# Kernel tuning notes

Hardware: AMD Instinct MI355X
Metric: run time of the kernel (lower is better)

The kernel has to match this reference:

```python
import jax, jax.numpy as jnp
import numpy as np


def binarize_ste(W):
    # sign binarization with straight-through estimator:
    # forward = sign(W) (zeros mapped to +1, standard BNN convention),
    # backward = identity.
    s = jnp.where(W >= 0, 1.0, -1.0).astype(W.dtype)
    return W + jax.lax.stop_gradient(s - W)


def setup_inputs() -> dict:
    key = jax.random.key(0)
    k1, k2 = jax.random.split(key)
    B, N_IN, N_UNITS = 4096, 4096, 4096
    x = jax.random.normal(k1, (B, N_IN), dtype=jnp.float32)
    W = jax.random.normal(k2, (N_IN, N_UNITS), dtype=jnp.float32) * 0.1  # truncated_normal(stddev=0.1) analog
    b = jnp.zeros((N_UNITS,), dtype=jnp.float32)  # constant_initializer(0.0)
    return {"x": x, "W": W, "b": b}


def reference(x, W, b):
    bin_w = binarize_ste(W)           # [n_in, n_units], values in {-1, +1}
    out = x @ bin_w + b               # dense GEMM + bias
    return jax.nn.relu(out)           # act
```

## Files before the change

kernel.cpp:

```cpp
#include <hip/hip_runtime.h>
#include <hip/hip_bf16.h>

typedef unsigned short u16;
typedef signed char i8;
typedef __attribute__((ext_vector_type(4))) int   int4v;
typedef __attribute__((ext_vector_type(4))) float f32x4;

#define GLOBAL_AS __attribute__((address_space(1)))
#define LDS_AS    __attribute__((address_space(3)))

__device__ __forceinline__ void gload_lds16(const void* g, void* l) {
    __builtin_amdgcn_global_load_lds((const GLOBAL_AS unsigned int*)g,
                                     (LDS_AS unsigned int*)l, 16, 0, 0);
}

__global__ __launch_bounds__(256) void quant_x_kernel(const float* __restrict__ X,
                                                      i8* __restrict__ Xq,
                                                      float* __restrict__ inv_s) {
    const int row = blockIdx.x;
    const int t   = threadIdx.x;
    const float4* src = (const float4*)(X + (size_t)row * 4096 + t * 16);
    float4 v0 = src[0], v1 = src[1], v2 = src[2], v3 = src[3];
    float vals[16] = {v0.x, v0.y, v0.z, v0.w, v1.x, v1.y, v1.z, v1.w,
                      v2.x, v2.y, v2.z, v2.w, v3.x, v3.y, v3.z, v3.w};
    float m = 0.f;
#pragma unroll
    for (int j = 0; j < 16; ++j) m = fmaxf(m, fabsf(vals[j]));
#pragma unroll
    for (int off = 32; off; off >>= 1) m = fmaxf(m, __shfl_xor(m, off));
    __shared__ float sm[4];
    if ((t & 63) == 0) sm[t >> 6] = m;
    __syncthreads();
    m = fmaxf(fmaxf(sm[0], sm[1]), fmaxf(sm[2], sm[3]));
    const float s = (m > 0.f) ? 127.0f / m : 0.f;
    uint4 packed;
    unsigned int* pw = (unsigned int*)&packed;
#pragma unroll
    for (int g = 0; g < 4; ++g) {
        unsigned int wd = 0;
#pragma unroll
        for (int j = 0; j < 4; ++j) {
            int q = (int)rintf(vals[g * 4 + j] * s);
            wd |= ((unsigned int)(q & 255)) << (8 * j);
        }
        pw[g] = wd;
    }
    ((uint4*)(Xq + (size_t)row * 4096))[t] = packed;
    if (t == 0) inv_s[row] = m * (1.0f / 127.0f);
}

__global__ __launch_bounds__(256) void conv_w_kernel(const float* __restrict__ W,
                                                     i8* __restrict__ Wt) {
    __shared__ __attribute__((aligned(16))) i8 tile[64][80];
    const int t  = threadIdx.x;
    const int k0 = (blockIdx.x & 63) * 64;
    const int n0 = (blockIdx.x >> 6) * 64;
#pragma unroll
    for (int i = 0; i < 4; ++i) {
        const int r = i * 16 + (t >> 4);
        const int c = (t & 15) * 4;
        float4 v = *(const float4*)&W[(size_t)(k0 + r) * 4096 + n0 + c];
        tile[c + 0][r] = (v.x >= 0.f) ? 1 : -1;
        tile[c + 1][r] = (v.y >= 0.f) ? 1 : -1;
        tile[c + 2][r] = (v.z >= 0.f) ? 1 : -1;
        tile[c + 3][r] = (v.w >= 0.f) ? 1 : -1;
    }
    __syncthreads();
    const int r = t >> 2;
    const int c = (t & 3) * 16;
    *(int4*)&Wt[(size_t)(n0 + r) * 4096 + k0 + c] = *(const int4*)&tile[r][c];
}


#define BAR()        __builtin_amdgcn_s_barrier()
#define LGKM0M()     asm volatile("s_waitcnt lgkmcnt(0)" ::: "memory")
#define WAIT_VM6()   asm volatile("s_waitcnt vmcnt(6)" ::: "memory")

#define STAGE_TILE(bufb, koff)                                                      \
    do {                                                                            \
        gload_lds16(AsrcT + (koff),                     lds + (bufb) + wA);         \
        gload_lds16(AsrcT + 65536 + (koff),             lds + (bufb) + wA + 1024);  \
        gload_lds16(BsrcT + (koff),                     lds + (bufb) + 8192 + wB);          \
        gload_lds16(BsrcT + 65536 + (koff),             lds + (bufb) + 8192 + wB + 1024);   \
        gload_lds16(BsrcT + 131072 + (koff),            lds + (bufb) + 8192 + wB + 2048);   \
        gload_lds16(BsrcT + 196608 + (koff),            lds + (bufb) + 8192 + wB + 3072);   \
    } while (0)

__global__ __launch_bounds__(256, 2) void gemm_bin_kernel(const i8* __restrict__ A,
                                                          const i8* __restrict__ Bt,
                                                          const float* __restrict__ bias,
                                                          const float* __restrict__ inv_s,
                                                          float* __restrict__ C) {
    __shared__ __attribute__((aligned(1024))) char lds[49152];

    const int bid = blockIdx.x;
    const int swz = (bid & 7) * 64 + (bid >> 3);
    const int bm  = swz >> 4;
    const int bn  = swz & 15;

    const int tid = threadIdx.x;
    const int w   = tid >> 6;
    const int l   = tid & 63;
    const int wm  = w >> 1;
    const int wn  = w & 1;

    const int lin8 = (l & 7) ^ (l >> 3);
    const int sr2  = (l >> 3) * 2 + (lin8 >> 2);
    const int sc   = (lin8 & 3) * 16;
    const char* AsrcT = (const char*)A  + (size_t)(bm * 128 + 32 * w + sr2) * 4096 + sc;
    const char* BsrcT = (const char*)Bt + (size_t)(bn * 256 + 64 * w + sr2) * 4096 + sc;
    const int wA = w * 2048;
    const int wB = w * 4096;

    const int rsl  = ((l >> 4) + 4 * (l & 1)) ^ ((l >> 1) & 7);
    const int a_rd = wm * 4096 + ((l & 15) >> 1) * 128 + rsl * 16;
    const int b_rd = 8192 + wn * 8192 + ((l & 15) >> 1) * 128 + rsl * 16;

    int4v acc[4][8] = {};
    int4v af[4], bf[8];

    STAGE_TILE(0, 0);
    STAGE_TILE(24576, 64);
    WAIT_VM6();
    BAR();

    for (int t = 0; t < 64; ++t) {
        const int bufb  = (t & 1) * 24576;
        const int koff2 = ((t + 2) & 63) * 64;

#pragma unroll
        for (int mi = 0; mi < 4; ++mi)
            af[mi] = *(const int4v*)(lds + bufb + a_rd + mi * 1024);
#pragma unroll
        for (int ni = 0; ni < 8; ++ni)
            bf[ni] = *(const int4v*)(lds + bufb + b_rd + ni * 1024);
        LGKM0M();
        BAR();
        STAGE_TILE(bufb, koff2);
        WAIT_VM6();
        BAR();

        __builtin_amdgcn_s_setprio(1);
#pragma unroll
        for (int mi = 0; mi < 4; ++mi)
#pragma unroll
            for (int ni = 0; ni < 8; ++ni)
                acc[mi][ni] = __builtin_amdgcn_mfma_i32_16x16x64_i8(af[mi], bf[ni],
                                                                    acc[mi][ni], 0, 0, 0);
        __builtin_amdgcn_s_setprio(0);
    }
    asm volatile("s_waitcnt vmcnt(0) lgkmcnt(0)" ::: "memory");

    const int col0 = bn * 256 + wn * 128 + (l & 15);
    const int row0 = bm * 128 + wm * 64 + ((l >> 4) << 2);
    float bn8[8];
#pragma unroll
    for (int ni = 0; ni < 8; ++ni) bn8[ni] = bias[col0 + ni * 16];
#pragma unroll
    for (int mi = 0; mi < 4; ++mi) {
#pragma unroll
        for (int r = 0; r < 4; ++r) {
            const int   grow = row0 + mi * 16 + r;
            const float ivs  = inv_s[grow];
#pragma unroll
            for (int ni = 0; ni < 8; ++ni) {
                const float v = (float)acc[mi][ni][r] * ivs + bn8[ni];
                C[(size_t)grow * 4096 + (col0 + ni * 16)] = v > 0.f ? v : 0.f;
            }
        }
    }
}

__global__ __launch_bounds__(256) void fallback_kernel(const float* __restrict__ X,
                                                       const float* __restrict__ W,
                                                       const float* __restrict__ b,
                                                       float* __restrict__ out) {
    __shared__ float xs[16][16];
    __shared__ float ws[16][17];
    const int row = blockIdx.y * 16 + threadIdx.y;
    const int col = blockIdx.x * 16 + threadIdx.x;
    float acc = 0.f;
    for (int k0 = 0; k0 < 4096; k0 += 16) {
        xs[threadIdx.y][threadIdx.x] = X[(size_t)row * 4096 + k0 + threadIdx.x];
        float w = W[(size_t)(k0 + threadIdx.y) * 4096 + col];
        ws[threadIdx.y][threadIdx.x] = (w >= 0.f) ? 1.f : -1.f;
        __syncthreads();
#pragma unroll
        for (int kk = 0; kk < 16; ++kk) acc += xs[threadIdx.y][kk] * ws[kk][threadIdx.x];
        __syncthreads();
    }
    const float v = acc + b[col];
    out[(size_t)row * 4096 + col] = v > 0.f ? v : 0.f;
}

extern "C" void kernel_launch(void* const* d_in, const int* in_sizes, int n_in,
                              void* d_out, int out_size, void* d_ws, size_t ws_size,
                              hipStream_t stream) {
    const float* x = (const float*)d_in[0];
    const float* W = (const float*)d_in[1];
    const float* b = (const float*)d_in[2];
    float* out = (float*)d_out;

    const size_t need = (size_t)32 * 1024 * 1024 + 64 * 1024;
    if (ws_size < need) {
        fallback_kernel<<<dim3(256, 256), dim3(16, 16), 0, stream>>>(x, W, b, out);
        return;
    }

    i8*    Xq  = (i8*)d_ws;
    i8*    Wt  = Xq + (size_t)4096 * 4096;
    float* ivs = (float*)(Xq + (size_t)2 * 4096 * 4096);

    quant_x_kernel<<<dim3(4096), dim3(256), 0, stream>>>(x, Xq, ivs);
    conv_w_kernel<<<dim3(4096), dim3(256), 0, stream>>>(W, Wt);
    gemm_bin_kernel<<<dim3(512), dim3(256), 0, stream>>>(Xq, Wt, b, ivs, out);
}
```

Before: 105.6 us.

## Enlarge GEMM block tile to 256x256 with 8 waves and triple-buffered LDS

The int8 GEMM block tile grows from 128x256 with 4 waves to 256x256 with 8 waves, so the launch becomes 256 blocks of 512 threads. The LDS pipeline moves from double buffering with two barriers per k-step to triple buffering with one barrier. Loads for step t+2 are issued before the current step's fragment reads. The aim is more data reuse per LDS and global byte and less synchronisation stall. In exchange, LDS use rises to 96 KB per block, occupancy is lower, and there is a single wave of 256 blocks.

```diff
diff --git a/kernel.cpp b/kernel.cpp
--- a/kernel.cpp
+++ b/kernel.cpp
@@ -74,98 +74,99 @@
 
 #define BAR()        __builtin_amdgcn_s_barrier()
 #define LGKM0M()     asm volatile("s_waitcnt lgkmcnt(0)" ::: "memory")
-#define WAIT_VM6()   asm volatile("s_waitcnt vmcnt(6)" ::: "memory")
-
-#define STAGE_TILE(bufb, koff)                                                      \
+#define WAIT_VM4()   asm volatile("s_waitcnt vmcnt(4)" ::: "memory")
+
+#define STAGE_TILE(base, koff)                                                      \
     do {                                                                            \
-        gload_lds16(AsrcT + (koff),                     lds + (bufb) + wA);         \
-        gload_lds16(AsrcT + 65536 + (koff),             lds + (bufb) + wA + 1024);  \
-        gload_lds16(BsrcT + (koff),                     lds + (bufb) + 8192 + wB);          \
-        gload_lds16(BsrcT + 65536 + (koff),             lds + (bufb) + 8192 + wB + 1024);   \
-        gload_lds16(BsrcT + 131072 + (koff),            lds + (bufb) + 8192 + wB + 2048);   \
-        gload_lds16(BsrcT + 196608 + (koff),            lds + (bufb) + 8192 + wB + 3072);   \
+        gload_lds16(AsrcT + (koff),         lds + (base) + wA);                     \
+        gload_lds16(AsrcT + 65536 + (koff), lds + (base) + wA + 1024);              \
+        gload_lds16(BsrcT + (koff),         lds + (base) + 16384 + wA);             \
+        gload_lds16(BsrcT + 65536 + (koff), lds + (base) + 16384 + wA + 1024);      \
     } while (0)
 
-__global__ __launch_bounds__(256, 2) void gemm_bin_kernel(const i8* __restrict__ A,
+__global__ __launch_bounds__(512, 2) void gemm_bin_kernel(const i8* __restrict__ A,
                                                           const i8* __restrict__ Bt,
                                                           const float* __restrict__ bias,
                                                           const float* __restrict__ inv_s,
                                                           float* __restrict__ C) {
-    __shared__ __attribute__((aligned(1024))) char lds[49152];
+    __shared__ __attribute__((aligned(1024))) char lds[98304];
 
     const int bid = blockIdx.x;
-    const int swz = (bid & 7) * 64 + (bid >> 3);
+    const int swz = (bid & 7) * 32 + (bid >> 3);
     const int bm  = swz >> 4;
     const int bn  = swz & 15;
 
     const int tid = threadIdx.x;
     const int w   = tid >> 6;
     const int l   = tid & 63;
-    const int wm  = w >> 1;
-    const int wn  = w & 1;
+    const int wm  = w >> 2;
+    const int wn  = w & 3;
 
     const int lin8 = (l & 7) ^ (l >> 3);
     const int sr2  = (l >> 3) * 2 + (lin8 >> 2);
     const int sc   = (lin8 & 3) * 16;
-    const char* AsrcT = (const char*)A  + (size_t)(bm * 128 + 32 * w + sr2) * 4096 + sc;
-    const char* BsrcT = (const char*)Bt + (size_t)(bn * 256 + 64 * w + sr2) * 4096 + sc;
+    const char* AsrcT = (const char*)A  + (size_t)(bm * 256 + 32 * w + sr2) * 4096 + sc;
+    const char* BsrcT = (const char*)Bt + (size_t)(bn * 256 + 32 * w + sr2) * 4096 + sc;
     const int wA = w * 2048;
-    const int wB = w * 4096;
 
     const int rsl  = ((l >> 4) + 4 * (l & 1)) ^ ((l >> 1) & 7);
-    const int a_rd = wm * 4096 + ((l & 15) >> 1) * 128 + rsl * 16;
-    const int b_rd = 8192 + wn * 8192 + ((l & 15) >> 1) * 128 + rsl * 16;
-
-    int4v acc[4][8] = {};
-    int4v af[4], bf[8];
+    const int a_rd = wm * 8192 + ((l & 15) >> 1) * 128 + rsl * 16;
+    const int b_rd = 16384 + wn * 4096 + ((l & 15) >> 1) * 128 + rsl * 16;
+
+    int4v acc[8][4] = {};
+    int4v af[8], bf[4];
 
     STAGE_TILE(0, 0);
-    STAGE_TILE(24576, 64);
-    WAIT_VM6();
+    STAGE_TILE(32768, 64);
+    WAIT_VM4();
     BAR();
 
+    int rb = 0;
+    int sb = 65536;
     for (int t = 0; t < 64; ++t) {
-        const int bufb  = (t & 1) * 24576;
         const int koff2 = ((t + 2) & 63) * 64;
 
-#pragma unroll
-        for (int mi = 0; mi < 4; ++mi)
-            af[mi] = *(const int4v*)(lds + bufb + a_rd + mi * 1024);
-#pragma unroll
-        for (int ni = 0; ni < 8; ++ni)
-            bf[ni] = *(const int4v*)(lds + bufb + b_rd + ni * 1024);
-        LGKM0M();
-        BAR();
-        STAGE_TILE(bufb, koff2);
-        WAIT_VM6();
-        BAR();
+        STAGE_TILE(sb, koff2);
+
+#pragma unroll
+        for (int mi = 0; mi < 8; ++mi)
+            af[mi] = *(const int4v*)(lds + rb + a_rd + mi * 1024);
+#pragma unroll
+        for (int ni = 0; ni < 4; ++ni)
+            bf[ni] = *(const int4v*)(lds + rb + b_rd + ni * 1024);
 
         __builtin_amdgcn_s_setprio(1);
 #pragma unroll
-        for (int mi = 0; mi < 4; ++mi)
-#pragma unroll
-            for (int ni = 0; ni < 8; ++ni)
+        for (int mi = 0; mi < 8; ++mi)
+#pragma unroll
+            for (int ni = 0; ni < 4; ++ni)
                 acc[mi][ni] = __builtin_amdgcn_mfma_i32_16x16x64_i8(af[mi], bf[ni],
                                                                     acc[mi][ni], 0, 0, 0);
         __builtin_amdgcn_s_setprio(0);
+
+        WAIT_VM4();
+        LGKM0M();
+        BAR();
+        sb = rb;
+        rb = (rb == 65536) ? 0 : rb + 32768;
     }
     asm volatile("s_waitcnt vmcnt(0) lgkmcnt(0)" ::: "memory");
 
-    const int col0 = bn * 256 + wn * 128 + (l & 15);
-    const int row0 = bm * 128 + wm * 64 + ((l >> 4) << 2);
-    float bn8[8];
-#pragma unroll
-    for (int ni = 0; ni < 8; ++ni) bn8[ni] = bias[col0 + ni * 16];
-#pragma unroll
-    for (int mi = 0; mi < 4; ++mi) {
+    const int col0 = bn * 256 + wn * 64 + (l & 15);
+    const int row0 = bm * 256 + wm * 128 + ((l >> 4) << 2);
+    float bn4[4];
+#pragma unroll
+    for (int n = 0; n < 4; ++n) bn4[n] = bias[col0 + n * 16];
+#pragma unroll
+    for (int m = 0; m < 8; ++m) {
 #pragma unroll
         for (int r = 0; r < 4; ++r) {
-            const int   grow = row0 + mi * 16 + r;
+            const int   grow = row0 + m * 16 + r;
             const float ivs  = inv_s[grow];
 #pragma unroll
-            for (int ni = 0; ni < 8; ++ni) {
-                const float v = (float)acc[mi][ni][r] * ivs + bn8[ni];
-                C[(size_t)grow * 4096 + (col0 + ni * 16)] = v > 0.f ? v : 0.f;
+            for (int n = 0; n < 4; ++n) {
+                const float v = (float)acc[m][n][r] * ivs + bn4[n];
+                C[(size_t)grow * 4096 + (col0 + n * 16)] = v > 0.f ? v : 0.f;
             }
         }
     }
@@ -213,5 +214,5 @@
 
     quant_x_kernel<<<dim3(4096), dim3(256), 0, stream>>>(x, Xq, ivs);
     conv_w_kernel<<<dim3(4096), dim3(256), 0, stream>>>(W, Wt);
-    gemm_bin_kernel<<<dim3(512), dim3(256), 0, stream>>>(Xq, Wt, b, ivs, out);
-}
+    gemm_bin_kernel<<<dim3(256), dim3(512), 0, stream>>>(Xq, Wt, b, ivs, out);
+}
```

After: 97.60 us. 7.5% less time.
